# Optimization experiments

Measured on AMD Instinct MI355X. Metric: run time of the kernel, lower is better.

## Reference

```python
import jax, jax.numpy as jnp
import numpy as np
import math

N, E, G = 10000, 100000, 500
HID, H = 128, 4
C = HID                      # out_channels per head (PyG TransformerConv)
NFREQ, NSPACE = 10, 3
EDIM = 2 * NFREQ * NSPACE    # 60 = dis_emb.dim
LAT, DIS = 6, 3
IN_DIM = HID + LAT + DIS     # 137
EPS = 1e-5


def _lin_init(k, fan_in, shape):
    b = 1.0 / math.sqrt(fan_in)
    return jax.random.uniform(k, shape, jnp.float32, -b, b)


def setup_inputs() -> dict:
    key = jax.random.key(0)
    ks = jax.random.split(key, 12)
    return dict(
        node_features=jax.random.normal(ks[0], (N, HID), jnp.float32),
        frac_coords=jax.random.uniform(ks[1], (N, DIS), jnp.float32),
        lattice_feats=jax.random.normal(ks[2], (G, LAT), jnp.float32),
        edge_index=jax.random.randint(ks[3], (2, E), 0, N),
        node2graph=jnp.sort(jax.random.randint(ks[4], (N,), 0, G)),
        frac_diff=jax.random.normal(ks[5], (E, DIS), jnp.float32) * 0.1,
        ln_gamma=jnp.ones((HID,), jnp.float32),
        ln_beta=jnp.zeros((HID,), jnp.float32),
        Wq=_lin_init(ks[6], IN_DIM, (IN_DIM, H * C)), bq=jnp.zeros((H * C,), jnp.float32),
        Wk=_lin_init(ks[7], IN_DIM, (IN_DIM, H * C)), bk=jnp.zeros((H * C,), jnp.float32),
        Wv=_lin_init(ks[8], IN_DIM, (IN_DIM, H * C)), bv=jnp.zeros((H * C,), jnp.float32),
        We=_lin_init(ks[9], EDIM, (EDIM, H * C)),
        Wskip=_lin_init(ks[10], IN_DIM, (IN_DIM, C)), bskip=jnp.zeros((C,), jnp.float32),
    )


def _sinusoids(frac_diff):
    # SinusoidsEmbedding: emb = x[...,None]*2*pi*arange(F); cat(sin, cos); detached
    freqs = 2.0 * jnp.pi * jnp.arange(NFREQ, dtype=jnp.float32)    # [F]
    emb = frac_diff[:, :, None] * freqs[None, None, :]             # [E,3,F]
    emb = emb.reshape(-1, NSPACE * NFREQ)                          # [E,30]
    return jnp.concatenate([jnp.sin(emb), jnp.cos(emb)], axis=-1)  # [E,60]


def _segment_softmax(scores, idx, num_segments):
    # softmax over variable-size neighborhoods grouped by target node idx
    m = jax.ops.segment_max(scores, idx, num_segments=num_segments)
    ex = jnp.exp(scores - m[idx])
    s = jax.ops.segment_sum(ex, idx, num_segments=num_segments)
    return ex / (s[idx] + 1e-16)


def reference(node_features, frac_coords, lattice_feats, edge_index, node2graph,
              frac_diff, ln_gamma, ln_beta, Wq, bq, Wk, bk, Wv, bv, We, Wskip, bskip):
    edge_emb = jax.lax.stop_gradient(_sinusoids(frac_diff))  # .detach() in original
    node_input = node_features
    # LayerNorm (biased variance, torch default)
    mu = node_features.mean(-1, keepdims=True)
    var = node_features.var(-1, keepdims=True)
    h = (node_features - mu) * jax.lax.rsqrt(var + EPS) * ln_gamma + ln_beta
    # gather per-graph lattice features to nodes, concat
    lat = lattice_feats.reshape(-1, LAT)[node2graph]                # [N,6]
    x = jnp.concatenate([h, lat, frac_coords], axis=1)              # [N,137]

    q = (x @ Wq + bq).reshape(N, H, C)
    k = (x @ Wk + bk).reshape(N, H, C)
    v = (x @ Wv + bv).reshape(N, H, C)
    e = (edge_emb @ We).reshape(E, H, C)                            # lin_edge (no bias)

    src, dst = edge_index[0], edge_index[1]  # message flows src -> dst (PyG default)
    k_e = k[src] + e                                                # [E,H,C]
    alpha = (q[dst] * k_e).sum(-1) / math.sqrt(C)                   # [E,H]
    alpha = _segment_softmax(alpha, dst, N)
    msg = (v[src] + e) * alpha[:, :, None]                          # [E,H,C]
    out = jax.ops.segment_sum(msg, dst, num_segments=N)             # [N,H,C]
    out = out.mean(axis=1)                                          # concat=False -> head mean
    out = out + (x @ Wskip + bskip)                                 # root skip connection
    return node_input + jax.nn.silu(out)
```

## Files before the change

kernel.cpp:

```cpp
#include <hip/hip_runtime.h>
#include <math.h>

#define N_NODES 10000
#define N_EDGES 100000
#define HIDDEN  128
#define NHEAD   4
#define CHAN    128
#define IN_DIM  137
#define KPAD    160
#define NCOLS   1904
#define NPAD    1920
#define LATD    6
#define DISD    3

#define PREP_BLOCKS 2500
#define TRANS_TILES 26
#define WQE_BLOCKS  150
#define WEBT_BLOCKS 128

#define SCAT_BLOCKS ((N_EDGES + 255) / 256)
#define GEMM_BX 15
#define GEMM_BY ((N_NODES + 63) / 64)
#define NR16    628
#define FRAG_STRIDE (5 * 64 * 8)

typedef __attribute__((ext_vector_type(8))) short short8v;
typedef __attribute__((ext_vector_type(4))) float float4v;
typedef __attribute__((ext_vector_type(2))) float float2v;

__device__ inline unsigned short f2bf(float f) {
    unsigned u = __float_as_uint(f);
    unsigned r = 0x7fffu + ((u >> 16) & 1u);
    return (unsigned short)((u + r) >> 16);
}
__device__ inline float bf2f(unsigned short u) {
    return __uint_as_float(((unsigned)u) << 16);
}
__device__ inline size_t frag_off(int grp16, int ks, int lane) {
    return (((size_t)grp16 * 5 + ks) * 64 + lane) * 8;
}
__device__ inline size_t frag_elem(int grp16, int lr, int k) {
    const int ks = k >> 5, g = (k >> 3) & 3, e = k & 7;
    return frag_off(grp16, ks, g * 16 + lr) + e;
}

__global__ __launch_bounds__(256) void prep_weights_kernel(
    const float* __restrict__ nf, const float* __restrict__ frac,
    const float* __restrict__ lat, const int* __restrict__ n2g,
    const float* __restrict__ gamma, const float* __restrict__ beta,
    const float* __restrict__ Wq, const float* __restrict__ bq,
    const float* __restrict__ Wk, const float* __restrict__ bk,
    const float* __restrict__ Wv, const float* __restrict__ bv,
    const float* __restrict__ Wsk, const float* __restrict__ bsk,
    const float* __restrict__ We,
    unsigned short* __restrict__ xfrag, int* __restrict__ hist,
    unsigned short* __restrict__ wfrag, float* __restrict__ bias_all,
    unsigned short* __restrict__ webt)
{
    __shared__ __align__(16) unsigned short Tlds[64 * 168];
    const int tid = threadIdx.x;

    if (blockIdx.x < PREP_BLOCKS) {
        int wave = tid >> 6;
        int lane = tid & 63;
        int n = blockIdx.x * 4 + wave;
        if (n >= N_NODES) return;

        float v0 = nf[n * HIDDEN + lane];
        float v1 = nf[n * HIDDEN + 64 + lane];
        float s  = v0 + v1;
        float sq = v0 * v0 + v1 * v1;
        #pragma unroll
        for (int m = 1; m < 64; m <<= 1) {
            s  += __shfl_xor(s, m);
            sq += __shfl_xor(sq, m);
        }
        float mean = s * (1.0f / 128.0f);
        float var  = sq * (1.0f / 128.0f) - mean * mean;
        float inv  = rsqrtf(var + 1e-5f);

        const int r16 = n >> 4, lr = n & 15;
        xfrag[frag_elem(r16, lr, lane)] =
            f2bf((v0 - mean) * inv * gamma[lane] + beta[lane]);
        xfrag[frag_elem(r16, lr, 64 + lane)] =
            f2bf((v1 - mean) * inv * gamma[64 + lane] + beta[64 + lane]);
        if (lane < LATD)
            xfrag[frag_elem(r16, lr, HIDDEN + lane)] = f2bf(lat[n2g[n] * LATD + lane]);
        if (lane < DISD)
            xfrag[frag_elem(r16, lr, HIDDEN + LATD + lane)] = f2bf(frac[n * DISD + lane]);
        if (lane >= 41)
            xfrag[frag_elem(r16, lr, 96 + lane)] = 0;
        if (lane == 0) hist[n] = 0;
    } else if (blockIdx.x < PREP_BLOCKS + TRANS_TILES) {
        const int n0 = (blockIdx.x - PREP_BLOCKS) * 64;
        for (int i = tid; i < 160 * 64; i += 256) {
            const int k = i >> 6, n = i & 63;
            const int col = n0 + n;
            float val = 0.0f;
            if (k < IN_DIM) {
                if (col < 512)        val = Wq[(size_t)k * 512 + col];
                else if (col < 1024)  val = Wk[(size_t)k * 512 + (col - 512)];
                else if (col < 1536)  val = Wv[(size_t)k * 512 + (col - 1024)];
                else                  val = Wsk[(size_t)k * 128 + (col - 1536)];
            }
            Tlds[n * 168 + k] = f2bf(val);
        }
        __syncthreads();
        for (int i = tid; i < 4 * 5 * 64; i += 256) {
            const int lane = i & 63;
            const int ks   = (i >> 6) % 5;
            const int c16l = i / (5 * 64);
            const int lr = lane & 15, g = lane >> 4;
            const int lcol = c16l * 16 + lr;
            const int k0 = ks * 32 + g * 8;
            const short8v v = *reinterpret_cast<const short8v*>(&Tlds[lcol * 168 + k0]);
            *reinterpret_cast<short8v*>(
                &wfrag[frag_off((n0 >> 4) + c16l, ks, lane)]) = v;
        }
        if (tid < 64) {
            const int col = n0 + tid;
            float b;
            if (col < 512)        b = bq[col];
            else if (col < 1024)  b = bk[col - 512];
            else if (col < 1536)  b = bv[col - 1024];
            else                  b = bsk[col - 1536];
            bias_all[col] = b;
        }
    } else if (blockIdx.x < PREP_BLOCKS + TRANS_TILES + WQE_BLOCKS) {
        int idx = (blockIdx.x - PREP_BLOCKS - TRANS_TILES) * 256 + tid;
        if (idx >= 240 * KPAD) return;
        int hj = idx / KPAD, k = idx % KPAD;
        int h = hj / 60, j = hj % 60;
        float s = 0.0f;
        if (k < IN_DIM) {
            #pragma unroll 4
            for (int c = 0; c < 128; ++c)
                s += Wq[(size_t)k * 512 + h * 128 + c] * We[(size_t)j * 512 + h * 128 + c];
        }
        const int col = 1664 + hj;
        wfrag[frag_elem(col >> 4, col & 15, k)] = f2bf(s);
        if (k == KPAD - 1) {
            float b = 0.0f;
            #pragma unroll 4
            for (int c = 0; c < 128; ++c)
                b += bq[h * 128 + c] * We[(size_t)j * 512 + h * 128 + c];
            bias_all[col] = b;
        }
    } else {
        int g = (blockIdx.x - PREP_BLOCKS - TRANS_TILES - WQE_BLOCKS) * 256 + tid;
        if (g >= 4 * 128 * 64) return;
        int h = g >> 13, c = (g >> 6) & 127, j = g & 63;
        float v = (j < 60) ? We[(size_t)j * 512 + h * 128 + c] : 0.0f;
        webt[g] = f2bf(v);
    }
}

__global__ __launch_bounds__(256) void hist_kernel(
    const int* __restrict__ eidx, int* __restrict__ hist)
{
    int e = blockIdx.x * 256 + threadIdx.x;
    if (e < N_EDGES) atomicAdd(&hist[eidx[N_EDGES + e]], 1);
}

__global__ __launch_bounds__(1024) void scan_kernel(
    const int* __restrict__ hist, int* __restrict__ offsets, int* __restrict__ cursor)
{
    __shared__ int part[1024];
    const int t = threadIdx.x;
    const int base = t * 10;
    int loc[10];
    int s = 0;
    #pragma unroll
    for (int i = 0; i < 10; ++i) {
        int v = (base + i < N_NODES) ? hist[base + i] : 0;
        loc[i] = s; s += v;
    }
    part[t] = s;
    __syncthreads();
    for (int off = 1; off < 1024; off <<= 1) {
        int v = (t >= off) ? part[t - off] : 0;
        __syncthreads();
        part[t] += v;
        __syncthreads();
    }
    int pre = (t > 0) ? part[t - 1] : 0;
    #pragma unroll
    for (int i = 0; i < 10; ++i)
        if (base + i < N_NODES) {
            offsets[base + i] = pre + loc[i];
            cursor[base + i]  = pre + loc[i];
        }
    if (t == 1023) offsets[N_NODES] = part[1023];
}

__global__ __launch_bounds__(256, 4) void gemm_scatter_kernel(
    const unsigned short* __restrict__ xfrag, const unsigned short* __restrict__ wfrag,
    const float* __restrict__ bias_all,
    const int* __restrict__ eidx, const float* __restrict__ fdiff,
    int* __restrict__ cursor, int* __restrict__ sorted_src,
    float* __restrict__ sorted_fd,
    float* __restrict__ sq, unsigned short* __restrict__ qbuf,
    unsigned char* __restrict__ kvb)
{
    if (blockIdx.x < SCAT_BLOCKS) {
        int e = blockIdx.x * 256 + threadIdx.x;
        if (e >= N_EDGES) return;
        int src = eidx[e];
        int dst = eidx[N_EDGES + e];
        int pos = atomicAdd(&cursor[dst], 1);
        sorted_src[pos] = src;
        sorted_fd[pos * 3 + 0] = fdiff[e * 3 + 0];
        sorted_fd[pos * 3 + 1] = fdiff[e * 3 + 1];
        sorted_fd[pos * 3 + 2] = fdiff[e * 3 + 2];
        return;
    }

    const int bx   = blockIdx.x - SCAT_BLOCKS;
    const int row0 = (bx / GEMM_BX) * 64;
    const int col0 = (bx % GEMM_BX) * 128;
    const int tid  = threadIdx.x;
    const int l    = tid & 63;
    const int wid  = tid >> 6;
    const int wr   = (wid >> 1) * 32;
    const int wc   = (wid & 1) * 64;
    const int lr   = l & 15;
    const int r16  = (row0 + wr) >> 4;
    const int c16  = (col0 + wc) >> 4;

    short8v a[2][5];
    #pragma unroll
    for (int ks = 0; ks < 5; ++ks)
        #pragma unroll
        for (int t = 0; t < 2; ++t)
            a[t][ks] = *reinterpret_cast<const short8v*>(
                &xfrag[frag_off(r16 + t, ks, l)]);

    float4v acc[2][4];
    #pragma unroll
    for (int tr = 0; tr < 2; ++tr)
        #pragma unroll
        for (int tc = 0; tc < 4; ++tc)
            acc[tr][tc] = (float4v){0.0f, 0.0f, 0.0f, 0.0f};

    #pragma unroll
    for (int ks = 0; ks < 5; ++ks) {
        short8v b[4];
        #pragma unroll
        for (int t = 0; t < 4; ++t)
            b[t] = *reinterpret_cast<const short8v*>(
                &wfrag[frag_off(c16 + t, ks, l)]);
        #pragma unroll
        for (int tr = 0; tr < 2; ++tr)
            #pragma unroll
            for (int tc = 0; tc < 4; ++tc)
                acc[tr][tc] = __builtin_amdgcn_mfma_f32_16x16x32_bf16(
                    a[tr][ks], b[tc], acc[tr][tc], 0, 0, 0);
    }

    #pragma unroll
    for (int tr = 0; tr < 2; ++tr) {
        #pragma unroll
        for (int tc = 0; tc < 4; ++tc) {
            const int col  = col0 + wc + tc * 16 + lr;
            const float bias = bias_all[col];
            #pragma unroll
            for (int j = 0; j < 4; ++j) {
                const int row = row0 + wr + tr * 16 + (l >> 4) * 4 + j;
                if (row < N_NODES) {
                    float val = acc[tr][tc][j] + bias;
                    if (col < 512) {
                        qbuf[(size_t)row * 512 + col] = f2bf(val);
                    } else if (col < 1024) {
                        const int h = (col - 512) >> 7, ck = (col - 512) & 127;
                        int p = __builtin_amdgcn_cvt_pk_fp8_f32(val, val, 0, false);
                        kvb[((size_t)row * 4 + h) * 256 + (ck >> 2) * 8 + (ck & 3)]
                            = (unsigned char)(p & 0xFF);
                    } else if (col < 1536) {
                        const int h = (col - 1024) >> 7, cv = (col - 1024) & 127;
                        int p = __builtin_amdgcn_cvt_pk_fp8_f32(val, val, 0, false);
                        kvb[((size_t)row * 4 + h) * 256 + (cv >> 2) * 8 + 4 + (cv & 3)]
                            = (unsigned char)(p & 0xFF);
                    } else if (col < 1664) {
                        sq[(size_t)row * 384 + (col - 1536)] = val;
                    } else if (col < NCOLS) {
                        sq[(size_t)row * 384 + 128 + (col - 1664)] = val;
                    }
                }
            }
        }
    }
}

__global__ __launch_bounds__(256) void gather_kernel(
    const float* __restrict__ sq, const unsigned short* __restrict__ qbuf,
    const unsigned char* __restrict__ kvb,
    const int* __restrict__ offsets, const int* __restrict__ sorted_src,
    const float* __restrict__ sorted_fd,
    unsigned short* __restrict__ avbh, unsigned short* __restrict__ aggbuf,
    float* __restrict__ sumwbuf)
{
    const int n    = blockIdx.x;
    const int h    = threadIdx.x >> 6;
    const int l    = threadIdx.x & 63;
    const int hl   = l & 31;
    const int half = l >> 5;
    const float TWO_PI = 6.283185307179586f;
    const float scale  = 0.08838834764831845f;

    const ushort4 qv = *reinterpret_cast<const ushort4*>(
        &qbuf[(size_t)n * 512 + h * 128 + 4 * hl]);
    const float q4x = bf2f(qv.x), q4y = bf2f(qv.y);
    const float q4z = bf2f(qv.z), q4w = bf2f(qv.w);
    const float qe_a = sq[(size_t)n * 384 + 128 + h * 60 + hl];
    const bool  v2ok = (hl < 28);
    const float qe_b = v2ok ? sq[(size_t)n * 384 + 128 + h * 60 + hl + 32] : 0.0f;

    const int   jj1  = (hl < 30) ? hl : hl - 30;
    const int   sd1  = jj1 / 10;
    const float fc1  = TWO_PI * (float)(jj1 % 10);
    const bool  sin1 = (hl < 30);
    const int   jj2  = hl + 2;
    const int   sd2  = v2ok ? (jj2 / 10) : 0;
    const float fc2  = v2ok ? TWO_PI * (float)(jj2 % 10) : 0.0f;

    float ax = 0.f, ay = 0.f, az = 0.f, aw = 0.f;
    float agg1 = 0.f, agg2 = 0.f, sumw = 0.f;
    const int e0 = offsets[n], e1 = offsets[n + 1];

    for (int base = e0; base < e1; base += 4) {
        const int eA = base + half;
        const int eB = base + half + 2;
        const bool okA = (eA < e1), okB = (eB < e1);
        const int iA = okA ? eA : e0;
        const int iB = okB ? eB : e0;
        const int srcA = sorted_src[iA];
        const int srcB = sorted_src[iB];
        const float fdA1 = sorted_fd[iA * 3 + sd1];
        const float fdA2 = sorted_fd[iA * 3 + sd2];
        const float fdB1 = sorted_fd[iB * 3 + sd1];
        const float fdB2 = sorted_fd[iB * 3 + sd2];
        const uint2 kvA = *reinterpret_cast<const uint2*>(
            kvb + ((size_t)srcA * 4 + h) * 256 + 8 * hl);
        const uint2 kvB = *reinterpret_cast<const uint2*>(
            kvb + ((size_t)srcB * 4 + h) * 256 + 8 * hl);

        const float eA1 = sin1 ? __sinf(fdA1 * fc1) : __cosf(fdA1 * fc1);
        const float eA2 = __cosf(fdA2 * fc2);
        const float eB1 = sin1 ? __sinf(fdB1 * fc1) : __cosf(fdB1 * fc1);
        const float eB2 = __cosf(fdB2 * fc2);

        const float2v kA01 = __builtin_amdgcn_cvt_pk_f32_fp8(kvA.x, false);
        const float2v kA23 = __builtin_amdgcn_cvt_pk_f32_fp8(kvA.x, true);
        const float2v kB01 = __builtin_amdgcn_cvt_pk_f32_fp8(kvB.x, false);
        const float2v kB23 = __builtin_amdgcn_cvt_pk_f32_fp8(kvB.x, true);

        float pAs = q4x * kA01[0] + q4y * kA01[1]
                  + q4z * kA23[0] + q4w * kA23[1]
                  + eA1 * qe_a + eA2 * qe_b;
        float pBs = q4x * kB01[0] + q4y * kB01[1]
                  + q4z * kB23[0] + q4w * kB23[1]
                  + eB1 * qe_a + eB2 * qe_b;
        #pragma unroll
        for (int m = 1; m <= 16; m <<= 1) {
            pAs += __shfl_xor(pAs, m);
            pBs += __shfl_xor(pBs, m);
        }
        const float wA = okA ? __expf(pAs * scale) : 0.0f;
        const float wB = okB ? __expf(pBs * scale) : 0.0f;
        sumw += wA + wB;

        const float2v vA01 = __builtin_amdgcn_cvt_pk_f32_fp8(kvA.y, false);
        const float2v vA23 = __builtin_amdgcn_cvt_pk_f32_fp8(kvA.y, true);
        const float2v vB01 = __builtin_amdgcn_cvt_pk_f32_fp8(kvB.y, false);
        const float2v vB23 = __builtin_amdgcn_cvt_pk_f32_fp8(kvB.y, true);
        ax += wA * vA01[0] + wB * vB01[0];
        ay += wA * vA01[1] + wB * vB01[1];
        az += wA * vA23[0] + wB * vB23[0];
        aw += wA * vA23[1] + wB * vB23[1];
        agg1 += wA * eA1 + wB * eB1;
        if (v2ok) agg2 += wA * eA2 + wB * eB2;
    }

    sumw += __shfl_xor(sumw, 32);
    ax += __shfl_xor(ax, 32);  ay += __shfl_xor(ay, 32);
    az += __shfl_xor(az, 32);  aw += __shfl_xor(aw, 32);
    agg1 += __shfl_xor(agg1, 32);
    agg2 += __shfl_xor(agg2, 32);

    if (half == 0) {
        ushort4 r;
        r.x = f2bf(ax); r.y = f2bf(ay); r.z = f2bf(az); r.w = f2bf(aw);
        *reinterpret_cast<ushort4*>(&avbh[(size_t)n * 512 + h * 128 + 4 * hl]) = r;
        aggbuf[n * 256 + h * 64 + hl]      = f2bf(agg1);
        aggbuf[n * 256 + h * 64 + 32 + hl] = f2bf(agg2);
        if (hl == 0) sumwbuf[n * 4 + h] = sumw;
    }
}

__global__ __launch_bounds__(256) void corrfin_kernel(
    const unsigned short* __restrict__ webt, const unsigned short* __restrict__ aggbuf,
    const unsigned short* __restrict__ avbh, const float* __restrict__ sumwbuf,
    const float* __restrict__ sq, const float* __restrict__ nf,
    float* __restrict__ out)
{
    const int node0 = blockIdx.x * 64;
    const int tid = threadIdx.x;
    const int l   = tid & 63;
    const int w   = tid >> 6;
    const int lr  = l & 15;
    const int lk  = (l >> 4) * 8;
    const int nbase = node0 + w * 16;

    float4v acc[4][8];
    #pragma unroll
    for (int h = 0; h < 4; ++h)
        #pragma unroll
        for (int nn = 0; nn < 8; ++nn)
            acc[h][nn] = (float4v){0.0f, 0.0f, 0.0f, 0.0f};

    const int arow = (nbase + lr < N_NODES) ? (nbase + lr) : 0;
    #pragma unroll
    for (int h = 0; h < 4; ++h) {
        #pragma unroll
        for (int ks = 0; ks < 2; ++ks) {
            const short8v a = *reinterpret_cast<const short8v*>(
                &aggbuf[(size_t)arow * 256 + h * 64 + ks * 32 + lk]);
            #pragma unroll
            for (int nn = 0; nn < 8; ++nn) {
                const short8v b = *reinterpret_cast<const short8v*>(
                    &webt[(size_t)(h * 128 + nn * 16 + lr) * 64 + ks * 32 + lk]);
                acc[h][nn] = __builtin_amdgcn_mfma_f32_16x16x32_bf16(a, b, acc[h][nn], 0, 0, 0);
            }
        }
    }

    float inv_sw[4][4];
    #pragma unroll
    for (int j = 0; j < 4; ++j) {
        const int node = nbase + (l >> 4) * 4 + j;
        const int nrd  = (node < N_NODES) ? node : 0;
        #pragma unroll
        for (int h = 0; h < 4; ++h)
            inv_sw[j][h] = 1.0f / (sumwbuf[nrd * 4 + h] + 1e-16f);
    }

    #pragma unroll
    for (int nn = 0; nn < 8; ++nn) {
        const int col = nn * 16 + lr;
        #pragma unroll
        for (int j = 0; j < 4; ++j) {
            const int node = nbase + (l >> 4) * 4 + j;
            if (node < N_NODES) {
                float z = 0.0f;
                #pragma unroll
                for (int h = 0; h < 4; ++h)
                    z += (bf2f(avbh[(size_t)node * 512 + h * 128 + col]) + acc[h][nn][j])
                         * inv_sw[j][h];
                z = 0.25f * z + sq[(size_t)node * 384 + col];
                float si = z / (1.0f + __expf(-z));
                out[node * CHAN + col] = nf[node * CHAN + col] + si;
            }
        }
    }
}

extern "C" void kernel_launch(void* const* d_in, const int* in_sizes, int n_in,
                              void* d_out, int out_size, void* d_ws, size_t ws_size,
                              hipStream_t stream)
{
    const float* nf    = (const float*)d_in[0];
    const float* frac  = (const float*)d_in[1];
    const float* lat   = (const float*)d_in[2];
    const int*   eidx  = (const int*)  d_in[3];
    const int*   n2g   = (const int*)  d_in[4];
    const float* fdiff = (const float*)d_in[5];
    const float* gamma = (const float*)d_in[6];
    const float* beta  = (const float*)d_in[7];
    const float* Wq    = (const float*)d_in[8];
    const float* bq    = (const float*)d_in[9];
    const float* Wk    = (const float*)d_in[10];
    const float* bk    = (const float*)d_in[11];
    const float* Wv    = (const float*)d_in[12];
    const float* bv    = (const float*)d_in[13];
    const float* We    = (const float*)d_in[14];
    const float* Wsk   = (const float*)d_in[15];
    const float* bsk   = (const float*)d_in[16];
    float* out = (float*)d_out;

    float* sq        = (float*)d_ws;
    float* sumwbuf   = sq + (size_t)N_NODES * 384;
    float* bias_all  = sumwbuf + (size_t)N_NODES * 4;
    float* sorted_fd = bias_all + NPAD;
    unsigned short* xfrag  = (unsigned short*)(sorted_fd + (size_t)N_EDGES * 3);
    unsigned short* wfrag  = xfrag + (size_t)NR16 * FRAG_STRIDE;
    unsigned short* webt   = wfrag + (size_t)(NPAD / 16) * FRAG_STRIDE;
    unsigned short* aggbuf = webt + 4 * 128 * 64;
    unsigned short* qbuf   = aggbuf + (size_t)N_NODES * 256;
    unsigned short* avbh   = qbuf + (size_t)N_NODES * 512;
    unsigned char*  kvb    = (unsigned char*)(avbh + (size_t)N_NODES * 512);
    int* hist       = (int*)(kvb + (size_t)N_NODES * 4 * 256);
    int* offsets    = hist + N_NODES;
    int* cursor     = offsets + N_NODES + 1;
    int* sorted_src = cursor + N_NODES;

    prep_weights_kernel<<<PREP_BLOCKS + TRANS_TILES + WQE_BLOCKS + WEBT_BLOCKS,
                          256, 0, stream>>>(
        nf, frac, lat, n2g, gamma, beta,
        Wq, bq, Wk, bk, Wv, bv, Wsk, bsk, We,
        xfrag, hist, wfrag, bias_all, webt);

    hist_kernel<<<(N_EDGES + 255) / 256, 256, 0, stream>>>(eidx, hist);
    scan_kernel<<<1, 1024, 0, stream>>>(hist, offsets, cursor);

    gemm_scatter_kernel<<<SCAT_BLOCKS + GEMM_BX * GEMM_BY, 256, 0, stream>>>(
        xfrag, wfrag, bias_all, eidx, fdiff, cursor, sorted_src, sorted_fd,
        sq, qbuf, kvb);

    gather_kernel<<<N_NODES, 256, 0, stream>>>(
        sq, qbuf, kvb, offsets, sorted_src, sorted_fd, avbh, aggbuf, sumwbuf);

    corrfin_kernel<<<(N_NODES + 63) / 64, 256, 0, stream>>>(
        webt, aggbuf, avbh, sumwbuf, sq, nf, out);
}
```

Before: 130.8 us.

## Widen gather lanes to 16-byte K/V loads, processing eight edges per iteration

The interleaved fp8 K/V buffer is relaid out in 8-byte K/V chunks so each lane loads a 16-byte uint4 covering 8 channels. Each head's 64 lanes now split into four quarters of 16 lanes, so eight edges are processed per loop iteration instead of four. The dot-product reduction needs four shuffle steps instead of five, and the edge embedding is spread as four terms per lane. This is meant to raise memory-level parallelism and cut per-edge instruction and shuffle overhead. The cost is more registers and a larger final cross-quarter reduction.

```diff
diff --git a/kernel.cpp b/kernel.cpp
--- a/kernel.cpp
+++ b/kernel.cpp
@@ -273,12 +273,12 @@
                     } else if (col < 1024) {
                         const int h = (col - 512) >> 7, ck = (col - 512) & 127;
                         int p = __builtin_amdgcn_cvt_pk_fp8_f32(val, val, 0, false);
-                        kvb[((size_t)row * 4 + h) * 256 + (ck >> 2) * 8 + (ck & 3)]
+                        kvb[((size_t)row * 4 + h) * 256 + (ck >> 3) * 16 + (ck & 7)]
                             = (unsigned char)(p & 0xFF);
                     } else if (col < 1536) {
                         const int h = (col - 1024) >> 7, cv = (col - 1024) & 127;
                         int p = __builtin_amdgcn_cvt_pk_fp8_f32(val, val, 0, false);
-                        kvb[((size_t)row * 4 + h) * 256 + (cv >> 2) * 8 + 4 + (cv & 3)]
+                        kvb[((size_t)row * 4 + h) * 256 + (cv >> 3) * 16 + 8 + (cv & 7)]
                             = (unsigned char)(p & 0xFF);
                     } else if (col < 1664) {
                         sq[(size_t)row * 384 + (col - 1536)] = val;
@@ -302,98 +302,124 @@
     const int n    = blockIdx.x;
     const int h    = threadIdx.x >> 6;
     const int l    = threadIdx.x & 63;
-    const int hl   = l & 31;
-    const int half = l >> 5;
+    const int ql   = l & 15;
+    const int quarter = l >> 4;
     const float TWO_PI = 6.283185307179586f;
     const float scale  = 0.08838834764831845f;
 
-    const ushort4 qv = *reinterpret_cast<const ushort4*>(
-        &qbuf[(size_t)n * 512 + h * 128 + 4 * hl]);
-    const float q4x = bf2f(qv.x), q4y = bf2f(qv.y);
-    const float q4z = bf2f(qv.z), q4w = bf2f(qv.w);
-    const float qe_a = sq[(size_t)n * 384 + 128 + h * 60 + hl];
-    const bool  v2ok = (hl < 28);
-    const float qe_b = v2ok ? sq[(size_t)n * 384 + 128 + h * 60 + hl + 32] : 0.0f;
-
-    const int   jj1  = (hl < 30) ? hl : hl - 30;
-    const int   sd1  = jj1 / 10;
-    const float fc1  = TWO_PI * (float)(jj1 % 10);
-    const bool  sin1 = (hl < 30);
-    const int   jj2  = hl + 2;
-    const int   sd2  = v2ok ? (jj2 / 10) : 0;
-    const float fc2  = v2ok ? TWO_PI * (float)(jj2 % 10) : 0.0f;
-
-    float ax = 0.f, ay = 0.f, az = 0.f, aw = 0.f;
-    float agg1 = 0.f, agg2 = 0.f, sumw = 0.f;
+    const uint4 qu = *reinterpret_cast<const uint4*>(
+        &qbuf[(size_t)n * 512 + h * 128 + 8 * ql]);
+    float q8[8];
+    q8[0] = bf2f((unsigned short)(qu.x & 0xffff)); q8[1] = bf2f((unsigned short)(qu.x >> 16));
+    q8[2] = bf2f((unsigned short)(qu.y & 0xffff)); q8[3] = bf2f((unsigned short)(qu.y >> 16));
+    q8[4] = bf2f((unsigned short)(qu.z & 0xffff)); q8[5] = bf2f((unsigned short)(qu.z >> 16));
+    q8[6] = bf2f((unsigned short)(qu.w & 0xffff)); q8[7] = bf2f((unsigned short)(qu.w >> 16));
+
+    bool  sint[4]; int sdt[4]; float fct[4], qet[4];
+    #pragma unroll
+    for (int t = 0; t < 4; ++t) {
+        const int j  = ql + 16 * t;
+        const bool ok = (j < 60);
+        const bool sn = (j < 30);
+        const int jj = sn ? j : j - 30;
+        int sd = jj / 10; if (sd > 2) sd = 2;
+        sint[t] = sn; sdt[t] = sd;
+        fct[t]  = TWO_PI * (float)(jj % 10);
+        qet[t]  = ok ? sq[(size_t)n * 384 + 128 + h * 60 + j] : 0.0f;
+    }
+
+    float av[8] = {0.f,0.f,0.f,0.f,0.f,0.f,0.f,0.f};
+    float agg[4] = {0.f,0.f,0.f,0.f};
+    float sumw = 0.f;
     const int e0 = offsets[n], e1 = offsets[n + 1];
 
-    for (int base = e0; base < e1; base += 4) {
-        const int eA = base + half;
-        const int eB = base + half + 2;
+    for (int base = e0; base < e1; base += 8) {
+        const int eA = base + quarter;
+        const int eB = base + quarter + 4;
         const bool okA = (eA < e1), okB = (eB < e1);
         const int iA = okA ? eA : e0;
         const int iB = okB ? eB : e0;
         const int srcA = sorted_src[iA];
         const int srcB = sorted_src[iB];
-        const float fdA1 = sorted_fd[iA * 3 + sd1];
-        const float fdA2 = sorted_fd[iA * 3 + sd2];
-        const float fdB1 = sorted_fd[iB * 3 + sd1];
-        const float fdB2 = sorted_fd[iB * 3 + sd2];
-        const uint2 kvA = *reinterpret_cast<const uint2*>(
-            kvb + ((size_t)srcA * 4 + h) * 256 + 8 * hl);
-        const uint2 kvB = *reinterpret_cast<const uint2*>(
-            kvb + ((size_t)srcB * 4 + h) * 256 + 8 * hl);
-
-        const float eA1 = sin1 ? __sinf(fdA1 * fc1) : __cosf(fdA1 * fc1);
-        const float eA2 = __cosf(fdA2 * fc2);
-        const float eB1 = sin1 ? __sinf(fdB1 * fc1) : __cosf(fdB1 * fc1);
-        const float eB2 = __cosf(fdB2 * fc2);
-
-        const float2v kA01 = __builtin_amdgcn_cvt_pk_f32_fp8(kvA.x, false);
-        const float2v kA23 = __builtin_amdgcn_cvt_pk_f32_fp8(kvA.x, true);
-        const float2v kB01 = __builtin_amdgcn_cvt_pk_f32_fp8(kvB.x, false);
-        const float2v kB23 = __builtin_amdgcn_cvt_pk_f32_fp8(kvB.x, true);
-
-        float pAs = q4x * kA01[0] + q4y * kA01[1]
-                  + q4z * kA23[0] + q4w * kA23[1]
-                  + eA1 * qe_a + eA2 * qe_b;
-        float pBs = q4x * kB01[0] + q4y * kB01[1]
-                  + q4z * kB23[0] + q4w * kB23[1]
-                  + eB1 * qe_a + eB2 * qe_b;
-        #pragma unroll
-        for (int m = 1; m <= 16; m <<= 1) {
-            pAs += __shfl_xor(pAs, m);
-            pBs += __shfl_xor(pBs, m);
-        }
-        const float wA = okA ? __expf(pAs * scale) : 0.0f;
-        const float wB = okB ? __expf(pBs * scale) : 0.0f;
+        float fdA[3], fdB[3];
+        fdA[0] = sorted_fd[iA * 3];     fdB[0] = sorted_fd[iB * 3];
+        fdA[1] = sorted_fd[iA * 3 + 1]; fdB[1] = sorted_fd[iB * 3 + 1];
+        fdA[2] = sorted_fd[iA * 3 + 2]; fdB[2] = sorted_fd[iB * 3 + 2];
+        const uint4 kvA = *reinterpret_cast<const uint4*>(
+            kvb + ((size_t)srcA * 4 + h) * 256 + 16 * ql);
+        const uint4 kvB = *reinterpret_cast<const uint4*>(
+            kvb + ((size_t)srcB * 4 + h) * 256 + 16 * ql);
+
+        float embA[4], embB[4];
+        #pragma unroll
+        for (int t = 0; t < 4; ++t) {
+            const float vA = fdA[sdt[t]] * fct[t];
+            const float vB = fdB[sdt[t]] * fct[t];
+            embA[t] = sint[t] ? __sinf(vA) : __cosf(vA);
+            embB[t] = sint[t] ? __sinf(vB) : __cosf(vB);
+        }
+
+        const float2v kA0 = __builtin_amdgcn_cvt_pk_f32_fp8(kvA.x, false);
+        const float2v kA1 = __builtin_amdgcn_cvt_pk_f32_fp8(kvA.x, true);
+        const float2v kA2 = __builtin_amdgcn_cvt_pk_f32_fp8(kvA.y, false);
+        const float2v kA3 = __builtin_amdgcn_cvt_pk_f32_fp8(kvA.y, true);
+        const float2v kB0 = __builtin_amdgcn_cvt_pk_f32_fp8(kvB.x, false);
+        const float2v kB1 = __builtin_amdgcn_cvt_pk_f32_fp8(kvB.x, true);
+        const float2v kB2 = __builtin_amdgcn_cvt_pk_f32_fp8(kvB.y, false);
+        const float2v kB3 = __builtin_amdgcn_cvt_pk_f32_fp8(kvB.y, true);
+
+        float pA = q8[0]*kA0[0] + q8[1]*kA0[1] + q8[2]*kA1[0] + q8[3]*kA1[1]
+                 + q8[4]*kA2[0] + q8[5]*kA2[1] + q8[6]*kA3[0] + q8[7]*kA3[1]
+                 + embA[0]*qet[0] + embA[1]*qet[1] + embA[2]*qet[2] + embA[3]*qet[3];
+        float pB = q8[0]*kB0[0] + q8[1]*kB0[1] + q8[2]*kB1[0] + q8[3]*kB1[1]
+                 + q8[4]*kB2[0] + q8[5]*kB2[1] + q8[6]*kB3[0] + q8[7]*kB3[1]
+                 + embB[0]*qet[0] + embB[1]*qet[1] + embB[2]*qet[2] + embB[3]*qet[3];
+        #pragma unroll
+        for (int m = 1; m <= 8; m <<= 1) {
+            pA += __shfl_xor(pA, m);
+            pB += __shfl_xor(pB, m);
+        }
+        const float wA = okA ? __expf(pA * scale) : 0.0f;
+        const float wB = okB ? __expf(pB * scale) : 0.0f;
         sumw += wA + wB;
 
-        const float2v vA01 = __builtin_amdgcn_cvt_pk_f32_fp8(kvA.y, false);
-        const float2v vA23 = __builtin_amdgcn_cvt_pk_f32_fp8(kvA.y, true);
-        const float2v vB01 = __builtin_amdgcn_cvt_pk_f32_fp8(kvB.y, false);
-        const float2v vB23 = __builtin_amdgcn_cvt_pk_f32_fp8(kvB.y, true);
-        ax += wA * vA01[0] + wB * vB01[0];
-        ay += wA * vA01[1] + wB * vB01[1];
-        az += wA * vA23[0] + wB * vB23[0];
-        aw += wA * vA23[1] + wB * vB23[1];
-        agg1 += wA * eA1 + wB * eB1;
-        if (v2ok) agg2 += wA * eA2 + wB * eB2;
-    }
-
-    sumw += __shfl_xor(sumw, 32);
-    ax += __shfl_xor(ax, 32);  ay += __shfl_xor(ay, 32);
-    az += __shfl_xor(az, 32);  aw += __shfl_xor(aw, 32);
-    agg1 += __shfl_xor(agg1, 32);
-    agg2 += __shfl_xor(agg2, 32);
-
-    if (half == 0) {
-        ushort4 r;
-        r.x = f2bf(ax); r.y = f2bf(ay); r.z = f2bf(az); r.w = f2bf(aw);
-        *reinterpret_cast<ushort4*>(&avbh[(size_t)n * 512 + h * 128 + 4 * hl]) = r;
-        aggbuf[n * 256 + h * 64 + hl]      = f2bf(agg1);
-        aggbuf[n * 256 + h * 64 + 32 + hl] = f2bf(agg2);
-        if (hl == 0) sumwbuf[n * 4 + h] = sumw;
+        const float2v vA0 = __builtin_amdgcn_cvt_pk_f32_fp8(kvA.z, false);
+        const float2v vA1 = __builtin_amdgcn_cvt_pk_f32_fp8(kvA.z, true);
+        const float2v vA2 = __builtin_amdgcn_cvt_pk_f32_fp8(kvA.w, false);
+        const float2v vA3 = __builtin_amdgcn_cvt_pk_f32_fp8(kvA.w, true);
+        const float2v vB0 = __builtin_amdgcn_cvt_pk_f32_fp8(kvB.z, false);
+        const float2v vB1 = __builtin_amdgcn_cvt_pk_f32_fp8(kvB.z, true);
+        const float2v vB2 = __builtin_amdgcn_cvt_pk_f32_fp8(kvB.w, false);
+        const float2v vB3 = __builtin_amdgcn_cvt_pk_f32_fp8(kvB.w, true);
+        av[0] += wA*vA0[0] + wB*vB0[0];  av[1] += wA*vA0[1] + wB*vB0[1];
+        av[2] += wA*vA1[0] + wB*vB1[0];  av[3] += wA*vA1[1] + wB*vB1[1];
+        av[4] += wA*vA2[0] + wB*vB2[0];  av[5] += wA*vA2[1] + wB*vB2[1];
+        av[6] += wA*vA3[0] + wB*vB3[0];  av[7] += wA*vA3[1] + wB*vB3[1];
+        #pragma unroll
+        for (int t = 0; t < 4; ++t)
+            agg[t] += wA * embA[t] + wB * embB[t];
+    }
+
+    #pragma unroll
+    for (int m = 16; m <= 32; m <<= 1) {
+        sumw += __shfl_xor(sumw, m);
+        #pragma unroll
+        for (int c = 0; c < 8; ++c) av[c] += __shfl_xor(av[c], m);
+        #pragma unroll
+        for (int t = 0; t < 4; ++t) agg[t] += __shfl_xor(agg[t], m);
+    }
+
+    if (quarter == 0) {
+        uint4 st;
+        st.x = (unsigned)f2bf(av[0]) | ((unsigned)f2bf(av[1]) << 16);
+        st.y = (unsigned)f2bf(av[2]) | ((unsigned)f2bf(av[3]) << 16);
+        st.z = (unsigned)f2bf(av[4]) | ((unsigned)f2bf(av[5]) << 16);
+        st.w = (unsigned)f2bf(av[6]) | ((unsigned)f2bf(av[7]) << 16);
+        *reinterpret_cast<uint4*>(&avbh[(size_t)n * 512 + h * 128 + 8 * ql]) = st;
+        #pragma unroll
+        for (int t = 0; t < 4; ++t)
+            aggbuf[n * 256 + h * 64 + ql + 16 * t] = f2bf(agg[t]);
+        if (ql == 0) sumwbuf[n * 4 + h] = sumw;
     }
 }
 
```

Result: slower. 134.3 us (+2.7%).
